# Kernel tuning notes

Measured on AMD Instinct MI355X. Metric: run time of the kernel, lower is better.

The kernel has to match this reference:

```python
import jax, jax.numpy as jnp
import numpy as np

ALPHA_LO = float(np.exp(-1.0 / 5.0))   # 0.8187
ALPHA_HI = float(np.exp(-1.0 / 25.0))  # 0.9608
BN_EPS = 1e-5

B, T, D_IN, H = 32, 2000, 512, 512


def setup_inputs() -> dict:
    key = jax.random.key(0)
    ks = jax.random.split(key, 5)
    x = jax.random.normal(ks[0], (B, T, D_IN), dtype=jnp.float32)
    W = jax.random.normal(ks[1], (H, D_IN), dtype=jnp.float32) / np.sqrt(D_IN)
    b = jax.random.normal(ks[2], (H,), dtype=jnp.float32) * 0.01
    alpha = jax.random.uniform(ks[3], (H,), dtype=jnp.float32,
                               minval=ALPHA_LO, maxval=ALPHA_HI)
    gamma = jnp.ones((H,), dtype=jnp.float32)
    beta = jnp.zeros((H,), dtype=jnp.float32)
    ut0 = jax.random.uniform(ks[4], (B, H), dtype=jnp.float32)
    return {"x": x, "W": W, "b": b, "alpha": alpha,
            "gamma": gamma, "beta": beta, "ut0": ut0}


def reference(x, W, b, alpha, gamma, beta, ut0):
    # Linear: [B,T,Din] @ [Din,H] + b
    Wx = jnp.einsum("btd,hd->bth", x, W) + b
    # BatchNorm1d (training forward): stats over flattened (B*T) dim
    flat = Wx.reshape(-1, Wx.shape[-1])
    mean = flat.mean(axis=0)
    var = flat.var(axis=0)  # biased, as torch BN uses for normalization
    Wx = ((flat - mean) * jax.lax.rsqrt(var + BN_EPS) * gamma + beta).reshape(Wx.shape)
    # Readout cell: leaky integration + softmax accumulation over time
    a = jnp.clip(alpha, ALPHA_LO, ALPHA_HI)

    def step(carry, wxt):
        ut, acc = carry
        ut = a * ut + (1.0 - a) * wxt          # [B,H]
        acc = acc + jax.nn.softmax(ut, axis=1)
        return (ut, acc), None

    wx_t = jnp.transpose(Wx, (1, 0, 2))  # [T,B,H]
    (_, out), _ = jax.lax.scan(step, (ut0, jnp.zeros_like(ut0)), wx_t)
    return out[:, None, :]  # [B,1,H]
```

## Files before the change

### kernel.cpp

```cpp
#include <hip/hip_runtime.h>
#include <hip/hip_bf16.h>
#include <stdint.h>


namespace {
constexpr int kB = 32;
constexpr int kT = 2000;
constexpr int kD = 512;
constexpr int kH = 512;
constexpr int kM = kB * kT;
constexpr int kL = 20;
constexpr int kC = kT / kL;
constexpr float kALo = 0.81873075307798182f;
constexpr float kAHi = 0.96078943915232320f;

typedef __bf16 bf16x4 __attribute__((ext_vector_type(4)));
typedef __bf16 bf16x8 __attribute__((ext_vector_type(8)));
typedef float floatx16 __attribute__((ext_vector_type(16)));

__device__ __forceinline__ float bf2f(unsigned short u) {
  return __builtin_bit_cast(float, (unsigned)u << 16);
}
__device__ __forceinline__ float clipa(float a) {
  return fminf(fmaxf(a, kALo), kAHi);
}
__device__ __forceinline__ float pow20(float a) {
  const float a2 = a * a, a4 = a2 * a2, a5 = a4 * a;
  const float a10 = a5 * a5;
  return a10 * a10;
}
__device__ __forceinline__ void gld_lds16(const void* g, void* l) {
  __builtin_amdgcn_global_load_lds(
      (const __attribute__((address_space(1))) uint32_t*)g,
      (__attribute__((address_space(3))) uint32_t*)(uintptr_t)l, 16, 0, 0);
}

__global__ __launch_bounds__(256) void wcvt_k(const float* __restrict__ W,
                                              __bf16* __restrict__ Wbf) {
  const int t = blockIdx.x * 256 + threadIdx.x;
  const float4 a0 = ((const float4*)W)[t * 2];
  const float4 a1 = ((const float4*)W)[t * 2 + 1];
  bf16x8 v;
  v[0] = (__bf16)a0.x; v[1] = (__bf16)a0.y; v[2] = (__bf16)a0.z; v[3] = (__bf16)a0.w;
  v[4] = (__bf16)a1.x; v[5] = (__bf16)a1.y; v[6] = (__bf16)a1.z; v[7] = (__bf16)a1.w;
  *(bf16x8*)(Wbf + (size_t)t * 8) = v;
}

__global__ __launch_bounds__(512, 2) void gemm_k(const float* __restrict__ X,
                                                 const __bf16* __restrict__ Wbf,
                                                 unsigned short* __restrict__ Wxb,
                                                 float* __restrict__ partial) {
  __shared__ __bf16 As[64][32];
  __shared__ __bf16 Bs[512][32];
  __shared__ float sred[2][kH];
  const int tid = threadIdx.x;
  const size_t row0 = (size_t)blockIdx.x * 64;
  const int w = tid >> 6, L = tid & 63;
  const int rt = w >> 2, ct0 = (w & 3) * 4;
  const int lhalf = L >> 5, l32 = L & 31;
  const int arow = tid >> 3, acol = (tid & 7) * 4;

  floatx16 acc[4] = {};
  const float* xbase = X + (row0 + arow) * kD + acol;
  float4 a_pre = *(const float4*)xbase;

#pragma unroll 1
  for (int s = 0; s < 16; ++s) {
    __syncthreads();
    bf16x4 av;
    av[0] = (__bf16)a_pre.x; av[1] = (__bf16)a_pre.y;
    av[2] = (__bf16)a_pre.z; av[3] = (__bf16)a_pre.w;
    *(bf16x4*)&As[arow][acol] = av;
    const int kk = s * 32;
#pragma unroll
    for (int j = 0; j < 4; ++j) {
      const int ci = j * 512 + w * 64 + L;
      const __bf16* src = Wbf + (size_t)(ci >> 2) * kD + kk + (ci & 3) * 8;
      gld_lds16(src, (char*)&Bs[0][0] + (size_t)ci * 16);
    }
    __syncthreads();
    if (s < 15) a_pre = *(const float4*)(xbase + (s + 1) * 32);
#pragma unroll
    for (int kh = 0; kh < 2; ++kh) {
      const bf16x8 af = *(const bf16x8*)&As[rt * 32 + l32][kh * 16 + lhalf * 8];
#pragma unroll
      for (int c = 0; c < 4; ++c) {
        const bf16x8 bfr = *(const bf16x8*)&Bs[(ct0 + c) * 32 + l32][kh * 16 + lhalf * 8];
        acc[c] = __builtin_amdgcn_mfma_f32_32x32x16_bf16(af, bfr, acc[c], 0, 0, 0);
      }
    }
  }

  __syncthreads();
  sred[0][tid] = 0.f;
  sred[1][tid] = 0.f;
  __syncthreads();
#pragma unroll
  for (int c = 0; c < 4; ++c) {
    float s = 0.f, q = 0.f;
#pragma unroll
    for (int r = 0; r < 16; ++r) {
      const float v = acc[c][r];
      s += v;
      q += v * v;
    }
    s += __shfl_xor(s, 32);
    q += __shfl_xor(q, 32);
    if (lhalf == 0) {
      atomicAdd(&sred[0][(ct0 + c) * 32 + l32], s);
      atomicAdd(&sred[1][(ct0 + c) * 32 + l32], q);
    }
  }
#pragma unroll
  for (int c = 0; c < 4; ++c) {
    const int col = (ct0 + c) * 32 + l32;
#pragma unroll
    for (int r = 0; r < 16; ++r) {
      const int row = rt * 32 + 4 * lhalf + (r & 3) + 8 * (r >> 2);
      const unsigned short u = __builtin_bit_cast(unsigned short, (__bf16)acc[c][r]);
      const unsigned un = __shfl_down((unsigned)u, 1);
      if ((l32 & 1) == 0)
        *(unsigned*)(Wxb + (row0 + row) * (size_t)kH + col) = (unsigned)u | (un << 16);
    }
  }
  __syncthreads();
  partial[(size_t)blockIdx.x * 1024 + tid] = sred[0][tid];
  partial[(size_t)blockIdx.x * 1024 + 512 + tid] = sred[1][tid];
}

__global__ __launch_bounds__(512) void red1_k(const float* __restrict__ partial,
                                              float* __restrict__ sums) {
  const int tid = threadIdx.x;
  const int r0 = blockIdx.x * 25;
  float s0 = 0.f, s1 = 0.f;
#pragma unroll 5
  for (int r = 0; r < 25; ++r) {
    s0 += partial[(size_t)(r0 + r) * 1024 + tid];
    s1 += partial[(size_t)(r0 + r) * 1024 + 512 + tid];
  }
  atomicAdd(&sums[tid], s0);
  atomicAdd(&sums[kH + tid], s1);
}

__global__ __launch_bounds__(512) void finalize_k(const float* __restrict__ sums,
                                                  const float* __restrict__ alpha,
                                                  const float* __restrict__ gamma,
                                                  const float* __restrict__ beta,
                                                  float* __restrict__ prm) {
  const int h = threadIdx.x;
  const float inv_n = 1.0f / (float)kM;
  const float mean = sums[h] * inv_n;
  const float var = sums[kH + h] * inv_n - mean * mean;
  const float sc = gamma[h] * rsqrtf(var + 1e-5f);
  const float sh = beta[h] - mean * sc;
  const float a = clipa(alpha[h]);
  prm[h] = sc;
  prm[kH + h] = sh;
  prm[2 * kH + h] = a;
  prm[3 * kH + h] = 1.0f - a;
  prm[4 * kH + h] = pow20(a);
}

__global__ __launch_bounds__(512) void agg_raw_k(const unsigned short* __restrict__ Wxb,
                                                 const float* __restrict__ alpha,
                                                 float* __restrict__ vbuf) {
  const int bc = blockIdx.x;
  const int b = bc / kC, c = bc % kC;
  const int h = threadIdx.x;
  const float a = clipa(alpha[h]);
  const float oma = 1.0f - a;
  const unsigned short* base = Wxb + ((size_t)b * kT + (size_t)c * kL) * kH + h;
  float v = 0.f;
#pragma unroll
  for (int i = 0; i < kL; ++i)
    v = a * v + oma * bf2f(base[(size_t)i * kH]);
  vbuf[(size_t)bc * kH + h] = v;
}

__global__ __launch_bounds__(512) void scan_k(const float* __restrict__ ut0,
                                              const float* __restrict__ alpha,
                                              const float* __restrict__ prm,
                                              float* __restrict__ vbuf) {
  const int b = blockIdx.x;
  const int h = threadIdx.x;
  const float a20 = pow20(clipa(alpha[h]));
  const float sc = prm[h];
  const float shc = prm[kH + h] * (1.0f - a20);
  float u = ut0[(size_t)b * kH + h];
  float vc[10];
#pragma unroll 1
  for (int cb = 0; cb < kC; cb += 10) {
#pragma unroll
    for (int j = 0; j < 10; ++j)
      vc[j] = vbuf[((size_t)b * kC + cb + j) * kH + h];
#pragma unroll
    for (int j = 0; j < 10; ++j) {
      vbuf[((size_t)b * kC + cb + j) * kH + h] = u;
      u = a20 * u + sc * vc[j] + shc;
    }
  }
}

__global__ __launch_bounds__(512) void soft_k(const unsigned short* __restrict__ Wxb,
                                              const float* __restrict__ prm,
                                              const float* __restrict__ ustart,
                                              float* __restrict__ accp) {
  __shared__ float part[kL][9];
  __shared__ float zinv[kL];
  const int bc = blockIdx.x;
  const int b = bc / kC, c = bc % kC;
  const int h = threadIdx.x;
  const int wv = h >> 6, lane = h & 63;
  const float sc = prm[h], sh = prm[kH + h];
  const float a = prm[2 * kH + h], oma = prm[3 * kH + h];
  float u = ustart[(size_t)bc * kH + h];
  const unsigned short* base = Wxb + ((size_t)b * kT + (size_t)c * kL) * kH + h;
  float e[kL];
#pragma unroll
  for (int i = 0; i < kL; ++i) {
    const float wvx = bf2f(base[(size_t)i * kH]) * sc + sh;
    u = a * u + oma * wvx;
    e[i] = __expf(u);
  }
#pragma unroll
  for (int i = 0; i < kL; ++i) {
    float s = e[i];
#pragma unroll
    for (int off = 32; off > 0; off >>= 1) s += __shfl_xor(s, off);
    if (lane == 0) part[i][wv] = s;
  }
  __syncthreads();
  if (h < kL) {
    float s = 0.f;
#pragma unroll
    for (int j = 0; j < 8; ++j) s += part[h][j];
    zinv[h] = 1.0f / s;
  }
  __syncthreads();
  float acc = 0.f;
#pragma unroll
  for (int i = 0; i < kL; ++i) acc += e[i] * zinv[i];
  accp[(size_t)bc * kH + h] = acc;
}

__global__ __launch_bounds__(512) void out_red_k(const float* __restrict__ accp,
                                                 float* __restrict__ out) {
  const int b = blockIdx.x;
  const int h = threadIdx.x;
  float s = 0.f;
#pragma unroll 4
  for (int c = 0; c < kC; ++c) s += accp[((size_t)b * kC + c) * kH + h];
  out[(size_t)b * kH + h] = s;
}

}

extern "C" void kernel_launch(void* const* d_in, const int* in_sizes, int n_in,
                              void* d_out, int out_size, void* d_ws, size_t ws_size,
                              hipStream_t stream) {
  const float* x = (const float*)d_in[0];
  const float* Wm = (const float*)d_in[1];
  const float* alpha = (const float*)d_in[3];
  const float* gamma = (const float*)d_in[4];
  const float* beta = (const float*)d_in[5];
  const float* ut0 = (const float*)d_in[6];
  float* out = (float*)d_out;

  float* wsp = (float*)d_ws;
  float* vbuf = wsp;
  float* accp = vbuf + (size_t)kB * kC * kH;
  float* partial = accp + (size_t)kB * kC * kH;
  float* sums = partial + (size_t)1000 * 1024;
  float* prm = sums + 2 * kH;
  __bf16* Wbf = (__bf16*)(prm + 5 * kH);
  unsigned short* Wxb = (unsigned short*)(Wbf + (size_t)kH * kD);

  hipMemsetAsync(sums, 0, 2 * kH * sizeof(float), stream);
  wcvt_k<<<128, 256, 0, stream>>>(Wm, Wbf);
  gemm_k<<<kM / 64, 512, 0, stream>>>(x, Wbf, Wxb, partial);
  agg_raw_k<<<kB * kC, 512, 0, stream>>>(Wxb, alpha, vbuf);
  red1_k<<<40, 512, 0, stream>>>(partial, sums);
  finalize_k<<<1, 512, 0, stream>>>(sums, alpha, gamma, beta, prm);
  scan_k<<<kB, 512, 0, stream>>>(ut0, alpha, prm, vbuf);
  soft_k<<<kB * kC, 512, 0, stream>>>(Wxb, prm, vbuf, accp);
  out_red_k<<<kB, 512, 0, stream>>>(accp, out);
}
```

Baseline: 320.7 us.

## Pre-permute bf16 W into k-chunk-major layout and use 2x2 MFMA warp tiles

The W conversion kernel now writes bf16 weights in a k-chunk-major order, so each GEMM stage loads one contiguous 32 KB block into LDS with linear addresses. The A tile in LDS is also stored k-quad-major, with a padding row to spread banks. Each wave now computes a 2x2 grid of 32x32 tiles instead of 1x4, which rebalances A and B fragment reuse and changes LDS read conflicts. This adds a strided scatter in the conversion kernel and changes the register layout of the accumulators.

```diff
diff --git a/kernel.cpp b/kernel.cpp
--- a/kernel.cpp
+++ b/kernel.cpp
@@ -43,24 +43,26 @@
   bf16x8 v;
   v[0] = (__bf16)a0.x; v[1] = (__bf16)a0.y; v[2] = (__bf16)a0.z; v[3] = (__bf16)a0.w;
   v[4] = (__bf16)a1.x; v[5] = (__bf16)a1.y; v[6] = (__bf16)a1.z; v[7] = (__bf16)a1.w;
-  *(bf16x8*)(Wbf + (size_t)t * 8) = v;
+  const int h = t >> 6, k8 = t & 63;
+  *(bf16x8*)(Wbf + ((size_t)k8 * 512 + h) * 8) = v;
 }
 
 __global__ __launch_bounds__(512, 2) void gemm_k(const float* __restrict__ X,
                                                  const __bf16* __restrict__ Wbf,
                                                  unsigned short* __restrict__ Wxb,
                                                  float* __restrict__ partial) {
-  __shared__ __bf16 As[64][32];
-  __shared__ __bf16 Bs[512][32];
+  __shared__ alignas(16) __bf16 As2[4][65][8];
+  __shared__ alignas(16) bf16x8 Bs2[2048];
   __shared__ float sred[2][kH];
   const int tid = threadIdx.x;
   const size_t row0 = (size_t)blockIdx.x * 64;
   const int w = tid >> 6, L = tid & 63;
-  const int rt = w >> 2, ct0 = (w & 3) * 4;
+  const int ct0 = w * 2;
   const int lhalf = L >> 5, l32 = L & 31;
   const int arow = tid >> 3, acol = (tid & 7) * 4;
-
-  floatx16 acc[4] = {};
+  const int akq = acol >> 3, aoff = acol & 7;
+
+  floatx16 acc[2][2] = {};
   const float* xbase = X + (row0 + arow) * kD + acol;
   float4 a_pre = *(const float4*)xbase;
 
@@ -70,24 +72,25 @@
     bf16x4 av;
     av[0] = (__bf16)a_pre.x; av[1] = (__bf16)a_pre.y;
     av[2] = (__bf16)a_pre.z; av[3] = (__bf16)a_pre.w;
-    *(bf16x4*)&As[arow][acol] = av;
-    const int kk = s * 32;
+    *(bf16x4*)&As2[akq][arow][aoff] = av;
 #pragma unroll
     for (int j = 0; j < 4; ++j) {
-      const int ci = j * 512 + w * 64 + L;
-      const __bf16* src = Wbf + (size_t)(ci >> 2) * kD + kk + (ci & 3) * 8;
-      gld_lds16(src, (char*)&Bs[0][0] + (size_t)ci * 16);
+      const int ci = j * 512 + tid;
+      gld_lds16(Wbf + ((size_t)s * 2048 + ci) * 8, (char*)&Bs2[0] + (size_t)ci * 16);
     }
     __syncthreads();
     if (s < 15) a_pre = *(const float4*)(xbase + (s + 1) * 32);
 #pragma unroll
     for (int kh = 0; kh < 2; ++kh) {
-      const bf16x8 af = *(const bf16x8*)&As[rt * 32 + l32][kh * 16 + lhalf * 8];
-#pragma unroll
-      for (int c = 0; c < 4; ++c) {
-        const bf16x8 bfr = *(const bf16x8*)&Bs[(ct0 + c) * 32 + l32][kh * 16 + lhalf * 8];
-        acc[c] = __builtin_amdgcn_mfma_f32_32x32x16_bf16(af, bfr, acc[c], 0, 0, 0);
-      }
+      const int kq = kh * 2 + lhalf;
+      const bf16x8 af0 = *(const bf16x8*)&As2[kq][l32][0];
+      const bf16x8 af1 = *(const bf16x8*)&As2[kq][32 + l32][0];
+      const bf16x8 b0 = Bs2[kq * 512 + ct0 * 32 + l32];
+      const bf16x8 b1 = Bs2[kq * 512 + (ct0 + 1) * 32 + l32];
+      acc[0][0] = __builtin_amdgcn_mfma_f32_32x32x16_bf16(af0, b0, acc[0][0], 0, 0, 0);
+      acc[0][1] = __builtin_amdgcn_mfma_f32_32x32x16_bf16(af0, b1, acc[0][1], 0, 0, 0);
+      acc[1][0] = __builtin_amdgcn_mfma_f32_32x32x16_bf16(af1, b0, acc[1][0], 0, 0, 0);
+      acc[1][1] = __builtin_amdgcn_mfma_f32_32x32x16_bf16(af1, b1, acc[1][1], 0, 0, 0);
     }
   }
 
@@ -96,13 +99,16 @@
   sred[1][tid] = 0.f;
   __syncthreads();
 #pragma unroll
-  for (int c = 0; c < 4; ++c) {
+  for (int c = 0; c < 2; ++c) {
     float s = 0.f, q = 0.f;
 #pragma unroll
-    for (int r = 0; r < 16; ++r) {
-      const float v = acc[c][r];
-      s += v;
-      q += v * v;
+    for (int rt = 0; rt < 2; ++rt) {
+#pragma unroll
+      for (int r = 0; r < 16; ++r) {
+        const float v = acc[rt][c][r];
+        s += v;
+        q += v * v;
+      }
     }
     s += __shfl_xor(s, 32);
     q += __shfl_xor(q, 32);
@@ -112,15 +118,18 @@
     }
   }
 #pragma unroll
-  for (int c = 0; c < 4; ++c) {
-    const int col = (ct0 + c) * 32 + l32;
-#pragma unroll
-    for (int r = 0; r < 16; ++r) {
-      const int row = rt * 32 + 4 * lhalf + (r & 3) + 8 * (r >> 2);
-      const unsigned short u = __builtin_bit_cast(unsigned short, (__bf16)acc[c][r]);
-      const unsigned un = __shfl_down((unsigned)u, 1);
-      if ((l32 & 1) == 0)
-        *(unsigned*)(Wxb + (row0 + row) * (size_t)kH + col) = (unsigned)u | (un << 16);
+  for (int rt = 0; rt < 2; ++rt) {
+#pragma unroll
+    for (int c = 0; c < 2; ++c) {
+      const int col = (ct0 + c) * 32 + l32;
+#pragma unroll
+      for (int r = 0; r < 16; ++r) {
+        const int row = rt * 32 + 4 * lhalf + (r & 3) + 8 * (r >> 2);
+        const unsigned short u = __builtin_bit_cast(unsigned short, (__bf16)acc[rt][c][r]);
+        const unsigned un = __shfl_down((unsigned)u, 1);
+        if ((l32 & 1) == 0)
+          *(unsigned*)(Wxb + (row0 + row) * (size_t)kH + col) = (unsigned)u | (un << 16);
+      }
     }
   }
   __syncthreads();
```

After: 308.9 us. 1.04x faster.
